# Performance work log

Measured on AMD Instinct MI355X. Metric: run time of the kernel, lower is better.

## Reference

```python
import jax, jax.numpy as jnp
import numpy as np

B, S, D = 2, 4096, 768
H, DH = 12, 64
W = 256          # one-sided window (attention_window=512 // 2)
G = 8            # number of global tokens (first G positions)
NEG = -1e9


def setup_inputs() -> dict:
    key = jax.random.key(0)
    ks = jax.random.split(key, 8)
    hidden_states = jax.random.normal(ks[0], (B, S, D), dtype=jnp.float32)
    attention_mask = jnp.ones((B, S), dtype=jnp.float32)
    sc = 0.02
    Wq = jax.random.normal(ks[1], (D, D), dtype=jnp.float32) * sc
    Wk = jax.random.normal(ks[2], (D, D), dtype=jnp.float32) * sc
    Wv = jax.random.normal(ks[3], (D, D), dtype=jnp.float32) * sc
    Wqg = jax.random.normal(ks[4], (D, D), dtype=jnp.float32) * sc
    Wkg = jax.random.normal(ks[5], (D, D), dtype=jnp.float32) * sc
    Wvg = jax.random.normal(ks[6], (D, D), dtype=jnp.float32) * sc
    return {"hidden_states": hidden_states, "attention_mask": attention_mask,
            "Wq": Wq, "Wk": Wk, "Wv": Wv, "Wqg": Wqg, "Wkg": Wkg, "Wvg": Wvg}


def _heads(x):  # [B,S,D] -> [B,H,S,DH]
    return x.reshape(B, S, H, DH).transpose(0, 2, 1, 3)


def longformer_attn(hidden_states, attention_mask, Wq, Wk, Wv, Wqg, Wkg, Wvg):
    scale = 1.0 / jnp.sqrt(jnp.float32(DH))
    q = _heads(hidden_states @ Wq) * scale   # [B,H,S,DH]
    k = _heads(hidden_states @ Wk)
    v = _heads(hidden_states @ Wv)

    n = S // W                                # number of query chunks
    kp = jnp.pad(k, ((0, 0), (0, 0), (W, W), (0, 0)))
    vp = jnp.pad(v, ((0, 0), (0, 0), (W, W), (0, 0)))
    # window indices into padded seq: chunk i covers keys [i*W - W, i*W + 2W)
    idx = jnp.arange(n)[:, None] * W + jnp.arange(3 * W)[None, :]   # [n,3W]
    k_win = kp[:, :, idx]                     # [B,H,n,3W,DH]
    v_win = vp[:, :, idx]
    qc = q.reshape(B, H, n, W, DH)

    scores = jnp.einsum('bhnqd,bhnkd->bhnqk', qc, k_win)  # [B,H,n,W,3W]

    # masks: band (|key-query|<=W), valid key position, not a global key,
    # and key attention_mask
    rel = jnp.arange(3 * W)[None, :] - jnp.arange(W)[:, None]   # [W,3W] = k - q
    band = (rel >= 0) & (rel <= 2 * W)
    key_pos = idx - W                                           # [n,3W] real positions
    valid = (key_pos >= 0) & (key_pos < S) & (key_pos >= G)
    struct_mask = band[None, :, :] & valid[:, None, :]          # [n,W,3W]
    amp = jnp.pad(attention_mask, ((0, 0), (W, W)))
    am_win = amp[:, idx] > 0.5                                  # [B,n,3W]
    full_mask = struct_mask[None] & am_win[:, :, None, :]       # [B,n,W,3W]
    scores = jnp.where(full_mask[:, None], scores, NEG)

    # every query also attends to the G global keys (regular key projection)
    gk = k[:, :, :G]                                            # [B,H,G,DH]
    gscore = jnp.einsum('bhsd,bhgd->bhsg', q, gk).reshape(B, H, n, W, G)
    all_scores = jnp.concatenate([gscore, scores], axis=-1)     # [B,H,n,W,G+3W]
    probs = jax.nn.softmax(all_scores, axis=-1)

    gv = v[:, :, :G]
    out = (jnp.einsum('bhnqk,bhnkd->bhnqd', probs[..., G:], v_win)
           + jnp.einsum('bhnqg,bhgd->bhnqd', probs[..., :G], gv))
    out = out.reshape(B, H, S, DH)

    # global queries attend to ALL tokens with the *_global projections
    qg = _heads(hidden_states @ Wqg)[:, :, :G] * scale          # [B,H,G,DH]
    kg = _heads(hidden_states @ Wkg)
    vg = _heads(hidden_states @ Wvg)
    gs = jnp.einsum('bhgd,bhsd->bhgs', qg, kg)                  # [B,H,G,S]
    gs = jnp.where(attention_mask[:, None, None, :] > 0.5, gs, NEG)
    gp = jax.nn.softmax(gs, axis=-1)
    gout = jnp.einsum('bhgs,bhsd->bhgd', gp, vg)
    out = out.at[:, :, :G].set(gout)

    return out.transpose(0, 2, 1, 3).reshape(B, S, D)


def reference(hidden_states, attention_mask, Wq, Wk, Wv, Wqg, Wkg, Wvg):
    return longformer_attn(hidden_states, attention_mask, Wq, Wk, Wv, Wqg, Wkg, Wvg)
```

## Files before the change

kernel.cpp:

```cpp
#include <hip/hip_runtime.h>

#define B_ 2
#define S_ 4096
#define D_ 768
#define H_ 12
#define DH_ 64
#define W_ 256
#define G_ 8
#define NEG_ (-1e9f)
#define NC_ 64
#define CK_ 64
#define WQB 64
#define NT_ 10

typedef __attribute__((ext_vector_type(4))) float f32x4;
typedef __attribute__((ext_vector_type(16))) float f32x16;
typedef __attribute__((ext_vector_type(8))) short s16x8;
typedef __attribute__((ext_vector_type(4))) short s16x4;
typedef unsigned short ushort_t;

__device__ __forceinline__ unsigned short f2bf(float f) {
    union { float f; unsigned u; } v; v.f = f;
    unsigned r = v.u + 0x7FFFu + ((v.u >> 16) & 1u);
    return (unsigned short)(r >> 16);
}
__device__ __forceinline__ float bf2f(unsigned short b) {
    union { unsigned u; float f; } v; v.u = ((unsigned)b) << 16;
    return v.f;
}
__device__ __forceinline__ unsigned cvtpk_bf16(float lo, float hi) {
    unsigned r;
    asm("v_cvt_pk_bf16_f32 %0, %1, %2" : "=v"(r) : "v"(lo), "v"(hi));
    return r;
}
__device__ __forceinline__ void gload16(const ushort_t* g, ushort_t* l) {
    __builtin_amdgcn_global_load_lds(
        (const __attribute__((address_space(1))) unsigned*)g,
        (__attribute__((address_space(3))) unsigned*)l, 16, 0, 0);
}
__device__ __forceinline__ float vmax16f(f32x16 v) {
    float a0 = fmaxf(v[0], v[1]), a1 = fmaxf(v[2], v[3]);
    float a2 = fmaxf(v[4], v[5]), a3 = fmaxf(v[6], v[7]);
    float a4 = fmaxf(v[8], v[9]), a5 = fmaxf(v[10], v[11]);
    float a6 = fmaxf(v[12], v[13]), a7 = fmaxf(v[14], v[15]);
    return fmaxf(fmaxf(fmaxf(a0, a1), fmaxf(a2, a3)),
                 fmaxf(fmaxf(a4, a5), fmaxf(a6, a7)));
}
__device__ __forceinline__ float vsum16f(f32x16 v) {
    float a0 = v[0] + v[1], a1 = v[2] + v[3];
    float a2 = v[4] + v[5], a3 = v[6] + v[7];
    float a4 = v[8] + v[9], a5 = v[10] + v[11];
    float a6 = v[12] + v[13], a7 = v[14] + v[15];
    return ((a0 + a1) + (a2 + a3)) + ((a4 + a5) + (a6 + a7));
}

__global__ __launch_bounds__(256) void fused_pre(const float* __restrict__ hs,
                                                 const float* __restrict__ W0,
                                                 const float* __restrict__ W1,
                                                 const float* __restrict__ W2,
                                                 const float* __restrict__ W3,
                                                 const float* __restrict__ W4,
                                                 const float* __restrict__ Wqg,
                                                 ushort_t* __restrict__ hs_bf,
                                                 ushort_t* __restrict__ wt,
                                                 float* __restrict__ qg) {
    __shared__ float smf[2 * D_];
    const int bid = blockIdx.x;
    const int t = threadIdx.x;

    if (bid < 3072) {
        const int i = bid * 256 + t;
        float4 a = *(const float4*)&hs[(size_t)i * 8];
        float4 c = *(const float4*)&hs[(size_t)i * 8 + 4];
        s16x8 o;
        o[0] = (short)f2bf(a.x); o[1] = (short)f2bf(a.y);
        o[2] = (short)f2bf(a.z); o[3] = (short)f2bf(a.w);
        o[4] = (short)f2bf(c.x); o[5] = (short)f2bf(c.y);
        o[6] = (short)f2bf(c.z); o[7] = (short)f2bf(c.w);
        *(s16x8*)&hs_bf[(size_t)i * 8] = o;
    } else if (bid < 5952) {
        const int bid2 = bid - 3072;
        const int w = bid2 / 576;
        const int rem = bid2 - w * 576;
        const int k0 = (rem / 24) * 32;
        const int n0 = (rem % 24) * 32;
        const float* Wsrc = (w == 0) ? W0 : (w == 1) ? W1 : (w == 2) ? W2 : (w == 3) ? W3 : W4;
        const float scl = (w == 0) ? 0.125f * 1.44269504f : 1.0f;
        const int r = t >> 3, c4 = (t & 7) * 4;
        float4 src = *(const float4*)&Wsrc[(size_t)(k0 + r) * D_ + n0 + c4];
        smf[r * 33 + c4 + 0] = src.x; smf[r * 33 + c4 + 1] = src.y;
        smf[r * 33 + c4 + 2] = src.z; smf[r * 33 + c4 + 3] = src.w;
        __syncthreads();
        s16x4 o;
        o[0] = (short)f2bf(smf[(c4 + 0) * 33 + r] * scl);
        o[1] = (short)f2bf(smf[(c4 + 1) * 33 + r] * scl);
        o[2] = (short)f2bf(smf[(c4 + 2) * 33 + r] * scl);
        o[3] = (short)f2bf(smf[(c4 + 3) * 33 + r] * scl);
        *(s16x4*)&wt[((size_t)(w * D_ + n0 + r)) * D_ + k0 + c4] = o;
    } else {
        const int bid3 = bid - 5952;
        const int rp = bid3 / 6;
        const int c0 = (bid3 - rp * 6) * 128;
        const int r = t >> 7, cl = t & 127;
        for (int i = t; i < 2 * D_; i += 256) {
            const int rr = i / D_, kk = i - rr * D_;
            const int row = rp * 2 + rr;
            const int b = row >> 3, g = row & 7;
            smf[rr * D_ + kk] = hs[((size_t)b * S_ + g) * D_ + kk];
        }
        __syncthreads();
        float a0 = 0.f, a1 = 0.f, a2 = 0.f, a3 = 0.f;
        const float* wp = &Wqg[c0 + cl];
        for (int kk = 0; kk < D_; kk += 4) {
            a0 += smf[r * D_ + kk + 0] * wp[(size_t)(kk + 0) * D_];
            a1 += smf[r * D_ + kk + 1] * wp[(size_t)(kk + 1) * D_];
            a2 += smf[r * D_ + kk + 2] * wp[(size_t)(kk + 2) * D_];
            a3 += smf[r * D_ + kk + 3] * wp[(size_t)(kk + 3) * D_];
        }
        const int row = rp * 2 + r;
        qg[(size_t)row * D_ + c0 + cl] = (a0 + a1 + a2 + a3) * 0.125f;
    }
}

__global__ __launch_bounds__(256, 2) void proj_mfma(const ushort_t* __restrict__ A,
                                                    const ushort_t* __restrict__ Bt,
                                                    ushort_t* __restrict__ oq,
                                                    ushort_t* __restrict__ ok,
                                                    ushort_t* __restrict__ ov,
                                                    ushort_t* __restrict__ okg,
                                                    ushort_t* __restrict__ ovg) {
    __shared__ char smem[34048];
    ushort_t* Al = (ushort_t*)smem;
    ushort_t* Bl = Al + 128 * 64;

    const int t = threadIdx.x;
    const int m0 = blockIdx.x * 128;
    const int n0 = blockIdx.y * 128;
    const int lane = t & 63;
    const int w = t >> 6;
    const int wm = (w >> 1) * 64, wn = (w & 1) * 64;
    const int ln = lane & 15, hi = lane >> 4;

    const int srow_in_call = lane >> 3;
    const int scol = ((lane & 7) ^ srow_in_call) * 8;

    f32x4 acc[4][4];
#pragma unroll
    for (int mi = 0; mi < 4; ++mi)
#pragma unroll
        for (int ni = 0; ni < 4; ++ni) acc[mi][ni] = (f32x4){0.f, 0.f, 0.f, 0.f};

    for (int k0 = 0; k0 < D_; k0 += 64) {
        __syncthreads();
#pragma unroll
        for (int j = 0; j < 4; ++j) {
            const int rbase = (w * 4 + j) * 8;
            const int row = rbase + srow_in_call;
            gload16(&A[(size_t)(m0 + row) * D_ + k0 + scol], &Al[rbase * 64]);
            gload16(&Bt[(size_t)(n0 + row) * D_ + k0 + scol], &Bl[rbase * 64]);
        }
        __syncthreads();

#pragma unroll
        for (int ks = 0; ks < 2; ++ks) {
            s16x8 af[4], bf[4];
#pragma unroll
            for (int i = 0; i < 4; ++i) {
                const int ar = wm + i * 16 + ln;
                const int br = wn + i * 16 + ln;
                const int slot = (4 * ks + hi) ^ (ln & 7);
                af[i] = *(const s16x8*)&Al[ar * 64 + slot * 8];
                bf[i] = *(const s16x8*)&Bl[br * 64 + slot * 8];
            }
#pragma unroll
            for (int mi = 0; mi < 4; ++mi)
#pragma unroll
                for (int ni = 0; ni < 4; ++ni)
                    acc[mi][ni] = __builtin_amdgcn_mfma_f32_16x16x32_bf16(af[mi], bf[ni], acc[mi][ni], 0, 0, 0);
        }
    }

    float* scr = (float*)smem;
    const int rl = t >> 2, cs = (t & 3) * 32;
    const int ng = n0 + cs;
    const int w_idx = ng / D_;
    const int cb = ng - w_idx * D_;
    const int hh = cb >> 6, dd = cb & 63;
    ushort_t* dst = (w_idx == 0) ? oq : (w_idx == 1) ? ok : (w_idx == 2) ? ov
                    : (w_idx == 3) ? okg : ovg;

#pragma unroll
    for (int r = 0; r < 2; ++r) {
        __syncthreads();
        if ((w >> 1) == r) {
#pragma unroll
            for (int mi = 0; mi < 4; ++mi)
#pragma unroll
                for (int ni = 0; ni < 4; ++ni)
#pragma unroll
                    for (int rr = 0; rr < 4; ++rr)
                        scr[(mi * 16 + hi * 4 + rr) * 132 + wn + ni * 16 + ln] = acc[mi][ni][rr];
        }
        __syncthreads();
        const int m = m0 + r * 64 + rl;
        const int bb = m >> 12, s = m & 4095;
        ushort_t* drow = dst + ((size_t)(bb * H_ + hh) * S_ + s) * DH_ + dd;
        const float* srcp = scr + rl * 132 + cs;
#pragma unroll
        for (int seg = 0; seg < 4; ++seg) {
            float4 lo = *(const float4*)&srcp[seg * 8];
            float4 hi4 = *(const float4*)&srcp[seg * 8 + 4];
            s16x8 o;
            o[0] = (short)f2bf(lo.x); o[1] = (short)f2bf(lo.y);
            o[2] = (short)f2bf(lo.z); o[3] = (short)f2bf(lo.w);
            o[4] = (short)f2bf(hi4.x); o[5] = (short)f2bf(hi4.y);
            o[6] = (short)f2bf(hi4.z); o[7] = (short)f2bf(hi4.w);
            *(s16x8*)&drow[seg * 8] = o;
        }
    }
}

__global__ __launch_bounds__(128, 2) void win_mfma(const ushort_t* __restrict__ q,
                                                   const ushort_t* __restrict__ k,
                                                   const ushort_t* __restrict__ v,
                                                   const float* __restrict__ am,
                                                   float* __restrict__ out) {
    __shared__ char smem[17680];
    ushort_t* Kl = (ushort_t*)smem;
    ushort_t* Vt = Kl + 64 * 72;
    unsigned* Mv = (unsigned*)(Vt + 64 * 66);
    float* Ow = (float*)smem;

    const int n = blockIdx.x, h = blockIdx.y, b = blockIdx.z;
    const int t = threadIdx.x;
    const int lane = t & 63, w = t >> 6;
    const int l31 = lane & 31, h5 = lane >> 5;
    const int q0w = n * WQB + w * 32;
    const int q_abs = q0w + l31;
    const size_t bh = (size_t)(b * H_ + h) * S_;

    s16x8 qf[4];
#pragma unroll
    for (int ks = 0; ks < 4; ++ks)
        qf[ks] = *(const s16x8*)&q[(bh + q_abs) * DH_ + ks * 16 + 8 * h5];

    f32x16 oacc[2];
#pragma unroll
    for (int dt = 0; dt < 2; ++dt)
#pragma unroll
        for (int i = 0; i < 16; ++i) oacc[dt][i] = 0.f;
    float m_run, l_run;

    const int srow = t >> 1, soff = (t & 1) * 32;
    s16x8 kr0, kr1, kr2, kr3, vr0, vr1, vr2, vr3;
    float amv = 0.f;

    {
        const ushort_t* krow = &k[(bh + srow) * DH_ + soff];
        kr0 = *(const s16x8*)krow;       kr1 = *(const s16x8*)(krow + 8);
        kr2 = *(const s16x8*)(krow + 16); kr3 = *(const s16x8*)(krow + 24);
        const ushort_t* vrow = &v[(bh + srow) * DH_ + soff];
        vr0 = *(const s16x8*)vrow;       vr1 = *(const s16x8*)(vrow + 8);
        vr2 = *(const s16x8*)(vrow + 16); vr3 = *(const s16x8*)(vrow + 24);
        *(s16x8*)&Kl[srow * 72 + soff] = kr0;
        *(s16x8*)&Kl[srow * 72 + soff + 8] = kr1;
        *(s16x8*)&Kl[srow * 72 + soff + 16] = kr2;
        *(s16x8*)&Kl[srow * 72 + soff + 24] = kr3;
#pragma unroll
        for (int i = 0; i < 8; ++i) {
            Vt[(soff + i) * 66 + srow] = (ushort_t)vr0[i];
            Vt[(soff + 8 + i) * 66 + srow] = (ushort_t)vr1[i];
            Vt[(soff + 16 + i) * 66 + srow] = (ushort_t)vr2[i];
            Vt[(soff + 24 + i) * 66 + srow] = (ushort_t)vr3[i];
        }
    }
    __syncthreads();

    {
        const int p = n * WQB - W_ + srow;
        const int pr = p < 0 ? 0 : p;
        const ushort_t* krow = &k[(bh + pr) * DH_ + soff];
        kr0 = *(const s16x8*)krow;       kr1 = *(const s16x8*)(krow + 8);
        kr2 = *(const s16x8*)(krow + 16); kr3 = *(const s16x8*)(krow + 24);
        const ushort_t* vrow = &v[(bh + pr) * DH_ + soff];
        vr0 = *(const s16x8*)vrow;       vr1 = *(const s16x8*)(vrow + 8);
        vr2 = *(const s16x8*)(vrow + 16); vr3 = *(const s16x8*)(vrow + 24);
        if (w == 0) {
            const int p2 = n * WQB - W_ + lane;
            amv = (p2 >= 0 && p2 < S_) ? am[(size_t)b * S_ + p2] : 0.f;
        }
    }

    {
        f32x16 s0;
#pragma unroll
        for (int i = 0; i < 16; ++i) s0[i] = 0.f;
#pragma unroll
        for (int ks = 0; ks < 4; ++ks) {
            s16x8 kf = *(const s16x8*)&Kl[l31 * 72 + ks * 16 + 8 * h5];
            s0 = __builtin_amdgcn_mfma_f32_32x32x16_bf16(kf, qf[ks], s0, 0, 0, 0);
        }
        float tmax = fmaxf(fmaxf(s0[0], s0[1]), fmaxf(s0[2], s0[3]));
        tmax = fmaxf(tmax, __shfl_xor(tmax, 32));
        m_run = tmax;
        float p0 = exp2f(s0[0] - m_run), p1 = exp2f(s0[1] - m_run);
        float p2 = exp2f(s0[2] - m_run), p3 = exp2f(s0[3] - m_run);
        float psum = (p0 + p1) + (p2 + p3);
        psum += __shfl_xor(psum, 32);
        l_run = psum;
        const unsigned Au = cvtpk_bf16(p0, p1);
        const unsigned Bu = cvtpk_bf16(p2, p3);
        const unsigned send0 = h5 ? Au : 0u;
        const unsigned send1 = h5 ? Bu : 0u;
        const unsigned recv0 = __shfl_xor((int)send0, 32);
        const unsigned recv1 = __shfl_xor((int)send1, 32);
        union { unsigned u[4]; s16x8 v8; } pu;
        pu.u[0] = h5 ? recv0 : Au;
        pu.u[1] = h5 ? recv1 : Bu;
        pu.u[2] = h5 ? 0u : recv0;
        pu.u[3] = h5 ? 0u : recv1;
#pragma unroll
        for (int dt = 0; dt < 2; ++dt) {
            const int vbase = (dt * 32 + l31) * 66 + 8 * h5;
            union { unsigned u[4]; s16x8 v8; } vf;
            vf.u[0] = *(const unsigned*)&Vt[vbase + 0];
            vf.u[1] = *(const unsigned*)&Vt[vbase + 2];
            vf.u[2] = *(const unsigned*)&Vt[vbase + 4];
            vf.u[3] = *(const unsigned*)&Vt[vbase + 6];
            oacc[dt] = __builtin_amdgcn_mfma_f32_32x32x16_bf16(vf.v8, pu.v8, oacc[dt], 0, 0, 0);
        }
    }

    for (int tt = 1; tt < NT_; ++tt) {
        const int pbase = n * WQB - W_ + (tt - 1) * 64;
        __syncthreads();
        *(s16x8*)&Kl[srow * 72 + soff] = kr0;
        *(s16x8*)&Kl[srow * 72 + soff + 8] = kr1;
        *(s16x8*)&Kl[srow * 72 + soff + 16] = kr2;
        *(s16x8*)&Kl[srow * 72 + soff + 24] = kr3;
#pragma unroll
        for (int i = 0; i < 8; ++i) {
            Vt[(soff + i) * 66 + srow] = (ushort_t)vr0[i];
            Vt[(soff + 8 + i) * 66 + srow] = (ushort_t)vr1[i];
            Vt[(soff + 16 + i) * 66 + srow] = (ushort_t)vr2[i];
            Vt[(soff + 24 + i) * 66 + srow] = (ushort_t)vr3[i];
        }
        if (w == 0) {
            const int p2 = pbase + lane;
            const bool ok = (p2 >= G_ && p2 < S_ && amv > 0.5f);
            unsigned long long bal = __ballot(ok);
            if (lane == 0) { Mv[0] = (unsigned)bal; Mv[1] = (unsigned)(bal >> 32); }
        }
        __syncthreads();

        if (tt < NT_ - 1) {
            const int p = pbase + 64 + srow;
            const int pr = p < 0 ? 0 : (p >= S_ ? S_ - 1 : p);
            const ushort_t* krow = &k[(bh + pr) * DH_ + soff];
            kr0 = *(const s16x8*)krow;       kr1 = *(const s16x8*)(krow + 8);
            kr2 = *(const s16x8*)(krow + 16); kr3 = *(const s16x8*)(krow + 24);
            const ushort_t* vrow = &v[(bh + pr) * DH_ + soff];
            vr0 = *(const s16x8*)vrow;       vr1 = *(const s16x8*)(vrow + 8);
            vr2 = *(const s16x8*)(vrow + 16); vr3 = *(const s16x8*)(vrow + 24);
            if (w == 0) {
                const int p2 = pbase + 64 + lane;
                amv = (p2 >= 0 && p2 < S_) ? am[(size_t)b * S_ + p2] : 0.f;
            }
        }

        f32x16 sc[2];
#pragma unroll
        for (int st = 0; st < 2; ++st)
#pragma unroll
            for (int i = 0; i < 16; ++i) sc[st][i] = 0.f;
#pragma unroll
        for (int st = 0; st < 2; ++st)
#pragma unroll
            for (int ks = 0; ks < 4; ++ks) {
                s16x8 kf = *(const s16x8*)&Kl[(st * 32 + l31) * 72 + ks * 16 + 8 * h5];
                sc[st] = __builtin_amdgcn_mfma_f32_32x32x16_bf16(kf, qf[ks], sc[st], 0, 0, 0);
            }

        const unsigned mv0 = Mv[0], mv1 = Mv[1];
        const bool fullt = ((mv0 & mv1) == 0xFFFFFFFFu) &&
                           (pbase >= q0w + 31 - W_) && (pbase + 63 <= q0w + W_);
        if (!fullt) {
#pragma unroll
            for (int st = 0; st < 2; ++st)
#pragma unroll
                for (int reg = 0; reg < 16; ++reg) {
                    const int cst = (reg & 3) + 8 * (reg >> 2);
                    const int crow = cst + 4 * h5;
                    const int key_abs = pbase + st * 32 + crow;
                    const unsigned mvx = (st == 0) ? mv0 : mv1;
                    const bool valid = ((mvx >> crow) & 1u) &&
                                       (key_abs >= q_abs - W_) && (key_abs <= q_abs + W_);
                    sc[st][reg] = valid ? sc[st][reg] : -1e30f;
                }
        }
        float tmax = fmaxf(vmax16f(sc[0]), vmax16f(sc[1]));
        tmax = fmaxf(tmax, __shfl_xor(tmax, 32));

        if (__any(tmax > m_run + 11.5f)) {
            const float mnew = fmaxf(m_run, tmax);
            const float f = exp2f(m_run - mnew);
            l_run *= f;
#pragma unroll
            for (int dt = 0; dt < 2; ++dt)
#pragma unroll
                for (int i = 0; i < 16; ++i) oacc[dt][i] *= f;
            m_run = mnew;
        }
#pragma unroll
        for (int st = 0; st < 2; ++st)
#pragma unroll
            for (int reg = 0; reg < 16; ++reg)
                sc[st][reg] = exp2f(sc[st][reg] - m_run);
        float psum = vsum16f(sc[0]) + vsum16f(sc[1]);
        psum += __shfl_xor(psum, 32);
        l_run += psum;

#pragma unroll
        for (int ks = 0; ks < 4; ++ks) {
            const int st = ks >> 1, k8 = (ks & 1) * 8;
            const unsigned Au = cvtpk_bf16(sc[st][k8 + 0], sc[st][k8 + 1]);
            const unsigned Bu = cvtpk_bf16(sc[st][k8 + 2], sc[st][k8 + 3]);
            const unsigned Cu = cvtpk_bf16(sc[st][k8 + 4], sc[st][k8 + 5]);
            const unsigned Du = cvtpk_bf16(sc[st][k8 + 6], sc[st][k8 + 7]);
            const unsigned send0 = h5 ? Au : Cu;
            const unsigned send1 = h5 ? Bu : Du;
            const unsigned recv0 = __shfl_xor((int)send0, 32);
            const unsigned recv1 = __shfl_xor((int)send1, 32);
            union { unsigned u[4]; s16x8 v8; } pu;
            pu.u[0] = h5 ? recv0 : Au;
            pu.u[1] = h5 ? recv1 : Bu;
            pu.u[2] = h5 ? Cu : recv0;
            pu.u[3] = h5 ? Du : recv1;
#pragma unroll
            for (int dt = 0; dt < 2; ++dt) {
                const int vbase = (dt * 32 + l31) * 66 + ks * 16 + 8 * h5;
                union { unsigned u[4]; s16x8 v8; } vf;
                vf.u[0] = *(const unsigned*)&Vt[vbase + 0];
                vf.u[1] = *(const unsigned*)&Vt[vbase + 2];
                vf.u[2] = *(const unsigned*)&Vt[vbase + 4];
                vf.u[3] = *(const unsigned*)&Vt[vbase + 6];
                oacc[dt] = __builtin_amdgcn_mfma_f32_32x32x16_bf16(vf.v8, pu.v8, oacc[dt], 0, 0, 0);
            }
        }
    }

    __syncthreads();
    const float inv = 1.0f / l_run;
    float* OwW = Ow + w * 32 * 68;
#pragma unroll
    for (int dt = 0; dt < 2; ++dt)
#pragma unroll
        for (int reg = 0; reg < 16; ++reg) {
            const int d = dt * 32 + (reg & 3) + 8 * (reg >> 2) + 4 * h5;
            OwW[l31 * 68 + d] = oacc[dt][reg] * inv;
        }
    asm volatile("s_waitcnt lgkmcnt(0)" ::: "memory");
    const int qq = lane >> 1, half = lane & 1;
    const float* src = &OwW[qq * 68 + half * 32];
    float* dstp = &out[((size_t)b * S_ + q0w + qq) * D_ + h * DH_ + half * 32];
#pragma unroll
    for (int j = 0; j < 8; ++j)
        *(float4*)&dstp[j * 4] = *(const float4*)&src[j * 4];
}

__global__ __launch_bounds__(256) void glob_partial(const float* __restrict__ qg,
                                                    const ushort_t* __restrict__ kg,
                                                    const ushort_t* __restrict__ vg,
                                                    const float* __restrict__ am,
                                                    float* __restrict__ pout,
                                                    float* __restrict__ pm,
                                                    float* __restrict__ pl) {
    const int c = blockIdx.x, h = blockIdx.y, b = blockIdx.z;
    const int t = threadIdx.x;
    const int bh = b * H_ + h;
    const size_t base = (size_t)bh * S_ * DH_;
    const int jg0 = c * CK_;

    __shared__ float qs[G_][DH_];
    __shared__ float kt[CK_][69];
    __shared__ float vt[CK_][68];
    __shared__ float ps[G_][CK_];

    for (int i = t; i < G_ * DH_; i += 256)
        qs[i >> 6][i & 63] = qg[(size_t)(b * G_ + (i >> 6)) * D_ + h * DH_ + (i & 63)];
    {
        const int row = t >> 2, off = (t & 3) * 16;
        const ushort_t* kr = &kg[base + (size_t)(jg0 + row) * DH_ + off];
        const ushort_t* vr = &vg[base + (size_t)(jg0 + row) * DH_ + off];
        s16x8 ka = *(const s16x8*)kr;
        s16x8 kb2 = *(const s16x8*)(kr + 8);
        s16x8 va = *(const s16x8*)vr;
        s16x8 vb = *(const s16x8*)(vr + 8);
#pragma unroll
        for (int i = 0; i < 8; ++i) {
            kt[row][off + i] = bf2f((ushort_t)ka[i]);
            kt[row][off + 8 + i] = bf2f((ushort_t)kb2[i]);
            vt[row][off + i] = bf2f((ushort_t)va[i]);
            vt[row][off + 8 + i] = bf2f((ushort_t)vb[i]);
        }
    }
    __syncthreads();

    const int g = t >> 5, jl = t & 31;
    float sc0 = 0.f, sc1 = 0.f;
#pragma unroll 8
    for (int d = 0; d < DH_; ++d) {
        const float qv = qs[g][d];
        sc0 += qv * kt[jl][d];
        sc1 += qv * kt[jl + 32][d];
    }
    if (!(am[(size_t)b * S_ + jg0 + jl] > 0.5f)) sc0 = NEG_;
    if (!(am[(size_t)b * S_ + jg0 + jl + 32] > 0.5f)) sc1 = NEG_;

    float mm = fmaxf(sc0, sc1);
    mm = fmaxf(mm, __shfl_xor(mm, 1));
    mm = fmaxf(mm, __shfl_xor(mm, 2));
    mm = fmaxf(mm, __shfl_xor(mm, 4));
    mm = fmaxf(mm, __shfl_xor(mm, 8));
    mm = fmaxf(mm, __shfl_xor(mm, 16));
    const float p0 = __expf(sc0 - mm);
    const float p1 = __expf(sc1 - mm);
    float ls = p0 + p1;
    ls += __shfl_xor(ls, 1);
    ls += __shfl_xor(ls, 2);
    ls += __shfl_xor(ls, 4);
    ls += __shfl_xor(ls, 8);
    ls += __shfl_xor(ls, 16);
    ps[g][jl] = p0;
    ps[g][jl + 32] = p1;
    if (jl == 0) {
        pm[((size_t)bh * NC_ + c) * G_ + g] = mm;
        pl[((size_t)bh * NC_ + c) * G_ + g] = ls;
    }
    __syncthreads();

#pragma unroll
    for (int pass = 0; pass < 2; ++pass) {
        const int gg = (t >> 6) + pass * 4;
        const int d = t & 63;
        float acc = 0.f;
#pragma unroll 8
        for (int j = 0; j < CK_; ++j) acc += ps[gg][j] * vt[j][d];
        pout[(((size_t)bh * NC_ + c) * G_ + gg) * DH_ + d] = acc;
    }
}

__global__ __launch_bounds__(256) void glob_reduce(const float* __restrict__ pout,
                                                   const float* __restrict__ pm,
                                                   const float* __restrict__ pl,
                                                   float* __restrict__ out) {
    const int bh = blockIdx.x;
    const int b = bh / H_, h = bh - b * H_;
    const int t = threadIdx.x;

    __shared__ float wc[G_][NC_];
    __shared__ float wsum[G_];

    const int g = t >> 5, cl = t & 31;
    const float m0 = pm[((size_t)bh * NC_ + cl) * G_ + g];
    const float m1 = pm[((size_t)bh * NC_ + cl + 32) * G_ + g];
    float M = fmaxf(m0, m1);
    M = fmaxf(M, __shfl_xor(M, 1));
    M = fmaxf(M, __shfl_xor(M, 2));
    M = fmaxf(M, __shfl_xor(M, 4));
    M = fmaxf(M, __shfl_xor(M, 8));
    M = fmaxf(M, __shfl_xor(M, 16));
    const float w0 = __expf(m0 - M);
    const float w1 = __expf(m1 - M);
    float S = w0 * pl[((size_t)bh * NC_ + cl) * G_ + g] +
              w1 * pl[((size_t)bh * NC_ + cl + 32) * G_ + g];
    S += __shfl_xor(S, 1);
    S += __shfl_xor(S, 2);
    S += __shfl_xor(S, 4);
    S += __shfl_xor(S, 8);
    S += __shfl_xor(S, 16);
    wc[g][cl] = w0;
    wc[g][cl + 32] = w1;
    if (cl == 0) wsum[g] = S;
    __syncthreads();

#pragma unroll
    for (int pass = 0; pass < 2; ++pass) {
        const int gg = (t >> 6) + pass * 4;
        const int d = t & 63;
        float acc = 0.f;
        for (int c2 = 0; c2 < NC_; ++c2)
            acc += wc[gg][c2] * pout[(((size_t)bh * NC_ + c2) * G_ + gg) * DH_ + d];
        out[((size_t)b * S_ + gg) * D_ + h * DH_ + d] = acc / wsum[gg];
    }
}

extern "C" void kernel_launch(void* const* d_in, const int* in_sizes, int n_in,
                              void* d_out, int out_size, void* d_ws, size_t ws_size,
                              hipStream_t stream) {
    (void)in_sizes; (void)n_in; (void)out_size; (void)ws_size;

    const float* hs    = (const float*)d_in[0];
    const float* amask = (const float*)d_in[1];
    const float* Wq    = (const float*)d_in[2];
    const float* Wk    = (const float*)d_in[3];
    const float* Wv    = (const float*)d_in[4];
    const float* Wqg   = (const float*)d_in[5];
    const float* Wkg   = (const float*)d_in[6];
    const float* Wvg   = (const float*)d_in[7];
    float* out = (float*)d_out;

    char* p = (char*)d_ws;
    ushort_t* hs_bf = (ushort_t*)p; p += (size_t)B_ * S_ * D_ * 2;
    ushort_t* wt    = (ushort_t*)p; p += (size_t)5 * D_ * D_ * 2;
    const size_t per = (size_t)B_ * H_ * S_ * DH_;
    ushort_t* qb  = (ushort_t*)p; p += per * 2;
    ushort_t* kb  = (ushort_t*)p; p += per * 2;
    ushort_t* vb  = (ushort_t*)p; p += per * 2;
    ushort_t* kgb = (ushort_t*)p; p += per * 2;
    ushort_t* vgb = (ushort_t*)p; p += per * 2;
    float* qg   = (float*)p; p += (size_t)B_ * G_ * D_ * 4;
    float* pout = (float*)p; p += (size_t)B_ * H_ * NC_ * G_ * DH_ * 4;
    float* pm   = (float*)p; p += (size_t)B_ * H_ * NC_ * G_ * 4;
    float* pl   = (float*)p;

    fused_pre<<<6000, 256, 0, stream>>>(hs, Wq, Wk, Wv, Wkg, Wvg, Wqg, hs_bf, wt, qg);
    proj_mfma<<<dim3(B_ * S_ / 128, 5 * D_ / 128), 256, 0, stream>>>(hs_bf, wt, qb, kb, vb, kgb, vgb);
    win_mfma<<<dim3(S_ / WQB, H_, B_), 128, 0, stream>>>(qb, kb, vb, amask, out);
    glob_partial<<<dim3(NC_, H_, B_), 256, 0, stream>>>(qg, kgb, vgb, amask, pout, pm, pl);
    glob_reduce<<<B_ * H_, 256, 0, stream>>>(pout, pm, pl, out);
}
```

Measured before the change: 161.0 us.

## Widen window-attention blocks to 128 queries and remove register prefetch

The windowed attention kernel now handles 128 queries per block with 4 waves (256 threads) instead of 64 with 2. Each K/V tile staged in shared memory is therefore shared by more queries, and the total number of blocks is halved. The register double-buffering prefetch is removed in favour of direct loads after the barrier. Waves now skip tiles that fall outside their band, and block IDs are remapped so neighbouring blocks fall on different XCDs. The cost is that global load latency is exposed, since loads are no longer overlapped with compute, and the larger shared-memory footprint and thread count may reduce occupancy.

Result: faster. 150.3 us (-6.7%).

```diff
diff --git a/kernel.cpp b/kernel.cpp
--- a/kernel.cpp
+++ b/kernel.cpp
@@ -10,8 +10,8 @@
 #define NEG_ (-1e9f)
 #define NC_ 64
 #define CK_ 64
-#define WQB 64
-#define NT_ 10
+#define WQB 128
+#define NT_ 11
 
 typedef __attribute__((ext_vector_type(4))) float f32x4;
 typedef __attribute__((ext_vector_type(16))) float f32x16;
@@ -220,18 +220,23 @@
     }
 }
 
-__global__ __launch_bounds__(128, 2) void win_mfma(const ushort_t* __restrict__ q,
+__global__ __launch_bounds__(256, 2) void win_mfma(const ushort_t* __restrict__ q,
                                                    const ushort_t* __restrict__ k,
                                                    const ushort_t* __restrict__ v,
                                                    const float* __restrict__ am,
                                                    float* __restrict__ out) {
-    __shared__ char smem[17680];
+    __shared__ char smem[34816];
     ushort_t* Kl = (ushort_t*)smem;
     ushort_t* Vt = Kl + 64 * 72;
     unsigned* Mv = (unsigned*)(Vt + 64 * 66);
     float* Ow = (float*)smem;
 
-    const int n = blockIdx.x, h = blockIdx.y, b = blockIdx.z;
+    const int bid = blockIdx.x;
+    const int wg = (bid & 7) * 96 + (bid >> 3);
+    const int n = wg & 31;
+    const int h = (wg >> 5) % H_;
+    const int b = wg / (32 * H_);
+
     const int t = threadIdx.x;
     const int lane = t & 63, w = t >> 6;
     const int l31 = lane & 31, h5 = lane >> 5;
@@ -251,45 +256,24 @@
         for (int i = 0; i < 16; ++i) oacc[dt][i] = 0.f;
     float m_run, l_run;
 
-    const int srow = t >> 1, soff = (t & 1) * 32;
-    s16x8 kr0, kr1, kr2, kr3, vr0, vr1, vr2, vr3;
-    float amv = 0.f;
+    const int srow = t >> 2, soff = (t & 3) * 16;
 
     {
         const ushort_t* krow = &k[(bh + srow) * DH_ + soff];
-        kr0 = *(const s16x8*)krow;       kr1 = *(const s16x8*)(krow + 8);
-        kr2 = *(const s16x8*)(krow + 16); kr3 = *(const s16x8*)(krow + 24);
+        s16x8 k0v = *(const s16x8*)krow;
+        s16x8 k1v = *(const s16x8*)(krow + 8);
+        *(s16x8*)&Kl[srow * 72 + soff] = k0v;
+        *(s16x8*)&Kl[srow * 72 + soff + 8] = k1v;
         const ushort_t* vrow = &v[(bh + srow) * DH_ + soff];
-        vr0 = *(const s16x8*)vrow;       vr1 = *(const s16x8*)(vrow + 8);
-        vr2 = *(const s16x8*)(vrow + 16); vr3 = *(const s16x8*)(vrow + 24);
-        *(s16x8*)&Kl[srow * 72 + soff] = kr0;
-        *(s16x8*)&Kl[srow * 72 + soff + 8] = kr1;
-        *(s16x8*)&Kl[srow * 72 + soff + 16] = kr2;
-        *(s16x8*)&Kl[srow * 72 + soff + 24] = kr3;
+        s16x8 v0v = *(const s16x8*)vrow;
+        s16x8 v1v = *(const s16x8*)(vrow + 8);
 #pragma unroll
         for (int i = 0; i < 8; ++i) {
-            Vt[(soff + i) * 66 + srow] = (ushort_t)vr0[i];
-            Vt[(soff + 8 + i) * 66 + srow] = (ushort_t)vr1[i];
-            Vt[(soff + 16 + i) * 66 + srow] = (ushort_t)vr2[i];
-            Vt[(soff + 24 + i) * 66 + srow] = (ushort_t)vr3[i];
+            Vt[(soff + i) * 66 + srow] = (ushort_t)v0v[i];
+            Vt[(soff + 8 + i) * 66 + srow] = (ushort_t)v1v[i];
         }
     }
     __syncthreads();
-
-    {
-        const int p = n * WQB - W_ + srow;
-        const int pr = p < 0 ? 0 : p;
-        const ushort_t* krow = &k[(bh + pr) * DH_ + soff];
-        kr0 = *(const s16x8*)krow;       kr1 = *(const s16x8*)(krow + 8);
-        kr2 = *(const s16x8*)(krow + 16); kr3 = *(const s16x8*)(krow + 24);
-        const ushort_t* vrow = &v[(bh + pr) * DH_ + soff];
-        vr0 = *(const s16x8*)vrow;       vr1 = *(const s16x8*)(vrow + 8);
-        vr2 = *(const s16x8*)(vrow + 16); vr3 = *(const s16x8*)(vrow + 24);
-        if (w == 0) {
-            const int p2 = n * WQB - W_ + lane;
-            amv = (p2 >= 0 && p2 < S_) ? am[(size_t)b * S_ + p2] : 0.f;
-        }
-    }
 
     {
         f32x16 s0;
@@ -334,39 +318,33 @@
     for (int tt = 1; tt < NT_; ++tt) {
         const int pbase = n * WQB - W_ + (tt - 1) * 64;
         __syncthreads();
-        *(s16x8*)&Kl[srow * 72 + soff] = kr0;
-        *(s16x8*)&Kl[srow * 72 + soff + 8] = kr1;
-        *(s16x8*)&Kl[srow * 72 + soff + 16] = kr2;
-        *(s16x8*)&Kl[srow * 72 + soff + 24] = kr3;
-#pragma unroll
-        for (int i = 0; i < 8; ++i) {
-            Vt[(soff + i) * 66 + srow] = (ushort_t)vr0[i];
-            Vt[(soff + 8 + i) * 66 + srow] = (ushort_t)vr1[i];
-            Vt[(soff + 16 + i) * 66 + srow] = (ushort_t)vr2[i];
-            Vt[(soff + 24 + i) * 66 + srow] = (ushort_t)vr3[i];
+        {
+            const int p = pbase + srow;
+            const int pr = p < 0 ? 0 : (p >= S_ ? S_ - 1 : p);
+            const ushort_t* krow = &k[(bh + pr) * DH_ + soff];
+            s16x8 k0v = *(const s16x8*)krow;
+            s16x8 k1v = *(const s16x8*)(krow + 8);
+            *(s16x8*)&Kl[srow * 72 + soff] = k0v;
+            *(s16x8*)&Kl[srow * 72 + soff + 8] = k1v;
+            const ushort_t* vrow = &v[(bh + pr) * DH_ + soff];
+            s16x8 v0v = *(const s16x8*)vrow;
+            s16x8 v1v = *(const s16x8*)(vrow + 8);
+#pragma unroll
+            for (int i = 0; i < 8; ++i) {
+                Vt[(soff + i) * 66 + srow] = (ushort_t)v0v[i];
+                Vt[(soff + 8 + i) * 66 + srow] = (ushort_t)v1v[i];
+            }
         }
         if (w == 0) {
             const int p2 = pbase + lane;
-            const bool ok = (p2 >= G_ && p2 < S_ && amv > 0.5f);
+            const bool ok = (p2 >= G_ && p2 < S_ && am[(size_t)b * S_ + (p2 < 0 ? 0 : (p2 >= S_ ? S_ - 1 : p2))] > 0.5f)
+                            && (p2 >= 0) && (p2 < S_);
             unsigned long long bal = __ballot(ok);
             if (lane == 0) { Mv[0] = (unsigned)bal; Mv[1] = (unsigned)(bal >> 32); }
         }
         __syncthreads();
 
-        if (tt < NT_ - 1) {
-            const int p = pbase + 64 + srow;
-            const int pr = p < 0 ? 0 : (p >= S_ ? S_ - 1 : p);
-            const ushort_t* krow = &k[(bh + pr) * DH_ + soff];
-            kr0 = *(const s16x8*)krow;       kr1 = *(const s16x8*)(krow + 8);
-            kr2 = *(const s16x8*)(krow + 16); kr3 = *(const s16x8*)(krow + 24);
-            const ushort_t* vrow = &v[(bh + pr) * DH_ + soff];
-            vr0 = *(const s16x8*)vrow;       vr1 = *(const s16x8*)(vrow + 8);
-            vr2 = *(const s16x8*)(vrow + 16); vr3 = *(const s16x8*)(vrow + 24);
-            if (w == 0) {
-                const int p2 = pbase + 64 + lane;
-                amv = (p2 >= 0 && p2 < S_) ? am[(size_t)b * S_ + p2] : 0.f;
-            }
-        }
+        if (pbase > q0w + 31 + W_ || pbase + 63 < q0w - W_) continue;
 
         f32x16 sc[2];
 #pragma unroll
@@ -626,7 +604,7 @@
 
     fused_pre<<<6000, 256, 0, stream>>>(hs, Wq, Wk, Wv, Wkg, Wvg, Wqg, hs_bf, wt, qg);
     proj_mfma<<<dim3(B_ * S_ / 128, 5 * D_ / 128), 256, 0, stream>>>(hs_bf, wt, qb, kb, vb, kgb, vgb);
-    win_mfma<<<dim3(S_ / WQB, H_, B_), 128, 0, stream>>>(qb, kb, vb, amask, out);
+    win_mfma<<<B_ * H_ * (S_ / WQB), 256, 0, stream>>>(qb, kb, vb, amask, out);
     glob_partial<<<dim3(NC_, H_, B_), 256, 0, stream>>>(qg, kgb, vgb, amask, pout, pm, pl);
     glob_reduce<<<B_ * H_, 256, 0, stream>>>(pout, pm, pl, out);
 }
```
